# Optimization experiments

Measured on AMD Instinct MI355X. Metric: run time of the kernel, lower is better.

The kernel has to match this reference:

```python
import jax, jax.numpy as jnp
import numpy as np

IN_Q = 256   # in_features // 4
OUT_Q = 256  # out_features // 4


def setup_inputs() -> dict:
    key = jax.random.key(0)
    kx, kr, ki, kj, kk = jax.random.split(key, 5)
    stdv = 1.0 / np.sqrt(IN_Q)
    return {
        "x": jax.random.normal(kx, (4, 8192, IN_Q * 4), dtype=jnp.float32),
        "r_weight": jax.random.uniform(kr, (OUT_Q, IN_Q), minval=-stdv, maxval=stdv, dtype=jnp.float32),
        "i_weight": jax.random.uniform(ki, (OUT_Q, IN_Q), minval=-stdv, maxval=stdv, dtype=jnp.float32),
        "j_weight": jax.random.uniform(kj, (OUT_Q, IN_Q), minval=-stdv, maxval=stdv, dtype=jnp.float32),
        "k_weight": jax.random.uniform(kk, (OUT_Q, IN_Q), minval=-stdv, maxval=stdv, dtype=jnp.float32),
        "bias": jnp.zeros((OUT_Q * 4,), dtype=jnp.float32),
    }


def reference(x, r_weight, i_weight, j_weight, k_weight, bias):
    batch_dims = x.shape[:-1]
    xq = x.reshape(*batch_dims, IN_Q, 4)  # [..., in_q, 4]
    r_x, i_x, j_x, k_x = xq[..., 0], xq[..., 1], xq[..., 2], xq[..., 3]

    lin = lambda v, w: jnp.einsum('...i,oi->...o', v, w)  # F.linear, no bias

    out_r = lin(r_x, r_weight) - lin(i_x, i_weight) - lin(j_x, j_weight) - lin(k_x, k_weight)
    out_i = lin(r_x, i_weight) + lin(i_x, r_weight) + lin(j_x, k_weight) - lin(k_x, j_weight)
    out_j = lin(r_x, j_weight) - lin(i_x, k_weight) + lin(j_x, r_weight) + lin(k_x, i_weight)
    out_k = lin(r_x, k_weight) + lin(i_x, j_weight) - lin(j_x, i_weight) + lin(k_x, r_weight)

    out = jnp.stack([out_r, out_i, out_j, out_k], axis=-1)  # [..., out_q, 4]
    out = out.reshape(*batch_dims, OUT_Q * 4)
    return out + bias
```

## Files before the change

### kernel.cpp

```cpp
#include <hip/hip_runtime.h>


typedef __attribute__((ext_vector_type(8))) short bf16x8;
typedef __attribute__((ext_vector_type(4))) float f32x4;

#define M_TOT 32768
#define N_TOT 1024
#define K_TOT 1024
#define BM 128
#define BN 128
#define BK 32

__device__ __forceinline__ unsigned short f2bf(float f) {
    union { float f; unsigned int u; } v; v.f = f;
    unsigned int u = v.u;
    u += 0x7fffu + ((u >> 16) & 1u);
    return (unsigned short)(u >> 16);
}

__global__ __launch_bounds__(256) void cvt_x(const float4* __restrict__ x,
                                             ushort4* __restrict__ y) {
    int idx = blockIdx.x * 256 + threadIdx.x;
    float4 a = x[idx];
    ushort4 o;
    o.x = f2bf(a.x); o.y = f2bf(a.y); o.z = f2bf(a.z); o.w = f2bf(a.w);
    y[idx] = o;
}

__global__ __launch_bounds__(256) void build_w(const float* __restrict__ R,
                                               const float* __restrict__ I,
                                               const float* __restrict__ J,
                                               const float* __restrict__ Kw,
                                               ushort4* __restrict__ Wb) {
    int n = blockIdx.x;
    int i = threadIdx.x;
    int o = n >> 2, co = n & 3;
    int base = o * 256 + i;
    float r = R[base], ii = I[base], j = J[base], k = Kw[base];
    float v0, v1, v2, v3;
    if (co == 0)      { v0 = r;  v1 = -ii; v2 = -j;  v3 = -k; }
    else if (co == 1) { v0 = ii; v1 = r;   v2 = k;   v3 = -j; }
    else if (co == 2) { v0 = j;  v1 = -k;  v2 = r;   v3 = ii; }
    else              { v0 = k;  v1 = j;   v2 = -ii; v3 = r;  }
    ushort4 w;
    w.x = f2bf(v0); w.y = f2bf(v1); w.z = f2bf(v2); w.w = f2bf(v3);
    Wb[n * 256 + i] = w;
}

__device__ __forceinline__ void async_lds16(const void* g, void* l) {
    __builtin_amdgcn_global_load_lds(
        (const __attribute__((address_space(1))) unsigned int*)g,
        (__attribute__((address_space(3))) unsigned int*)l,
        16, 0, 0);
}

__global__ __launch_bounds__(256) void gemm_bt(
        const unsigned short* __restrict__ A,
        const unsigned short* __restrict__ B,
        const float* __restrict__ bias,
        float* __restrict__ C) {
    __shared__ unsigned short As[BM * BK];
    __shared__ unsigned short Bs[BN * BK];

    const int tid  = threadIdx.x;
    const int wave = tid >> 6;
    const int lane = tid & 63;
    const int quad = lane >> 4;
    const int r16  = lane & 15;
    const int wm   = wave & 1;
    const int wn   = wave >> 1;

    const int m0 = blockIdx.x * BM;
    const int n0 = blockIdx.y * BN;

    f32x4 acc[4][4];
#pragma unroll
    for (int i = 0; i < 4; ++i)
#pragma unroll
        for (int j = 0; j < 4; ++j)
            acc[i][j] = (f32x4){0.f, 0.f, 0.f, 0.f};

    const int srow = lane >> 2;
    const int scol = (lane & 3) * 8;

    for (int k0 = 0; k0 < K_TOT; k0 += BK) {
        __syncthreads();
#pragma unroll
        for (int j = 0; j < 2; ++j) {
            int q   = wave * 2 + j;
            int row = q * 16 + srow;
            async_lds16(A + (size_t)(m0 + row) * K_TOT + k0 + scol, As + q * 512);
            async_lds16(B + (size_t)(n0 + row) * K_TOT + k0 + scol, Bs + q * 512);
        }
        __syncthreads();

        bf16x8 af[4], bf[4];
#pragma unroll
        for (int i = 0; i < 4; ++i) {
            af[i] = *(const bf16x8*)(As + (wm * 64 + i * 16 + r16) * BK + quad * 8);
            bf[i] = *(const bf16x8*)(Bs + (wn * 64 + i * 16 + r16) * BK + quad * 8);
        }
#pragma unroll
        for (int i = 0; i < 4; ++i)
#pragma unroll
            for (int j = 0; j < 4; ++j)
                acc[i][j] = __builtin_amdgcn_mfma_f32_16x16x32_bf16(
                    af[i], bf[j], acc[i][j], 0, 0, 0);
    }

#pragma unroll
    for (int j = 0; j < 4; ++j) {
        int col  = n0 + wn * 64 + j * 16 + r16;
        float bv = bias[col];
#pragma unroll
        for (int i = 0; i < 4; ++i) {
            int rowb = m0 + wm * 64 + i * 16 + quad * 4;
            f32x4 v  = acc[i][j];
#pragma unroll
            for (int r = 0; r < 4; ++r)
                C[(size_t)(rowb + r) * N_TOT + col] = v[r] + bv;
        }
    }
}

extern "C" void kernel_launch(void* const* d_in, const int* in_sizes, int n_in,
                              void* d_out, int out_size, void* d_ws, size_t ws_size,
                              hipStream_t stream) {
    const float* x    = (const float*)d_in[0];
    const float* rw   = (const float*)d_in[1];
    const float* iw   = (const float*)d_in[2];
    const float* jw   = (const float*)d_in[3];
    const float* kw   = (const float*)d_in[4];
    const float* bias = (const float*)d_in[5];
    float* out = (float*)d_out;

    unsigned short* xb = (unsigned short*)d_ws;
    unsigned short* Wb = (unsigned short*)((char*)d_ws + (size_t)M_TOT * K_TOT * 2);

    cvt_x<<<(M_TOT * (size_t)K_TOT) / 4 / 256, 256, 0, stream>>>(
        (const float4*)x, (ushort4*)xb);

    build_w<<<N_TOT, 256, 0, stream>>>(rw, iw, jw, kw, (ushort4*)Wb);

    dim3 grid(M_TOT / BM, N_TOT / BN);
    gemm_bt<<<grid, 256, 0, stream>>>(xb, Wb, bias, out);
}
```

Baseline: 327.4 us.

## Rewrite GEMM as 256x256 double-buffered pipelined kernel with swizzled LDS

Replaces the 128x128x32 single-buffered GEMM with a 256x256x64 tile and 512 threads. LDS is double-buffered, with async global-to-LDS prefetch of the next K tiles interleaved between four MFMA phases. The LDS layout is XOR-swizzled to avoid bank conflicts, s_setprio prioritizes the MFMA sections, and a block-ID remap groups tiles for L2 reuse. The goal is to hide load latency and cut the per-tile barrier stalls. In exchange it adds heavy register pressure from 32 accumulators and intricate vmcnt/barrier bookkeeping that is hard to get right.

```diff
diff --git a/kernel.cpp b/kernel.cpp
--- a/kernel.cpp
+++ b/kernel.cpp
@@ -7,9 +7,10 @@
 #define M_TOT 32768
 #define N_TOT 1024
 #define K_TOT 1024
-#define BM 128
-#define BN 128
-#define BK 32
+#define BM 256
+#define BN 256
+#define BK 64
+#define NKT (K_TOT / BK)
 
 __device__ __forceinline__ unsigned short f2bf(float f) {
     union { float f; unsigned int u; } v; v.f = f;
@@ -54,13 +55,34 @@
         16, 0, 0);
 }
 
-__global__ __launch_bounds__(256) void gemm_bt(
+__device__ __forceinline__ void stage_ht(const unsigned short* __restrict__ G,
+                                         int row0, int k0,
+                                         unsigned short* ht,
+                                         int wave, int lane) {
+    int sr = lane >> 2;
+    int sc = ((lane & 3) * 8) ^ ((lane & 32) ? 16 : 0);
+#pragma unroll
+    for (int j = 0; j < 2; ++j) {
+        int si = j * 8 + wave;
+        int rg = si >> 1, cg = si & 1;
+        async_lds16(G + (size_t)(row0 + rg * 16 + sr) * K_TOT + k0 + cg * 32 + sc,
+                    ht + si * 512);
+    }
+}
+
+__device__ __forceinline__ bf16x8 frag_ld(const unsigned short* ht,
+                                          int row, int kk, int quad) {
+    int idx = (((row >> 4) << 1) + (kk >> 5)) * 512 + (row & 15) * 32 + quad * 8;
+    idx ^= (row & 8) << 1;
+    return *(const bf16x8*)(ht + idx);
+}
+
+__global__ __launch_bounds__(512, 2) void gemm_bt(
         const unsigned short* __restrict__ A,
         const unsigned short* __restrict__ B,
         const float* __restrict__ bias,
         float* __restrict__ C) {
-    __shared__ unsigned short As[BM * BK];
-    __shared__ unsigned short Bs[BN * BK];
+    __shared__ unsigned short smem[2][2][2][8192];
 
     const int tid  = threadIdx.x;
     const int wave = tid >> 6;
@@ -70,52 +92,140 @@
     const int wm   = wave & 1;
     const int wn   = wave >> 1;
 
-    const int m0 = blockIdx.x * BM;
-    const int n0 = blockIdx.y * BN;
-
-    f32x4 acc[4][4];
-#pragma unroll
-    for (int i = 0; i < 4; ++i)
+    int bid = blockIdx.x;
+    int wg  = (bid & 7) * 64 + (bid >> 3);
+    const int m0 = (wg >> 2) * BM;
+    const int n0 = (wg & 3) * BN;
+
+    f32x4 acc[8][4];
+#pragma unroll
+    for (int i = 0; i < 8; ++i)
 #pragma unroll
         for (int j = 0; j < 4; ++j)
             acc[i][j] = (f32x4){0.f, 0.f, 0.f, 0.f};
 
-    const int srow = lane >> 2;
-    const int scol = (lane & 3) * 8;
-
-    for (int k0 = 0; k0 < K_TOT; k0 += BK) {
-        __syncthreads();
-#pragma unroll
-        for (int j = 0; j < 2; ++j) {
-            int q   = wave * 2 + j;
-            int row = q * 16 + srow;
-            async_lds16(A + (size_t)(m0 + row) * K_TOT + k0 + scol, As + q * 512);
-            async_lds16(B + (size_t)(n0 + row) * K_TOT + k0 + scol, Bs + q * 512);
-        }
-        __syncthreads();
-
-        bf16x8 af[4], bf[4];
-#pragma unroll
-        for (int i = 0; i < 4; ++i) {
-            af[i] = *(const bf16x8*)(As + (wm * 64 + i * 16 + r16) * BK + quad * 8);
-            bf[i] = *(const bf16x8*)(Bs + (wn * 64 + i * 16 + r16) * BK + quad * 8);
-        }
-#pragma unroll
-        for (int i = 0; i < 4; ++i)
-#pragma unroll
-            for (int j = 0; j < 4; ++j)
-                acc[i][j] = __builtin_amdgcn_mfma_f32_16x16x32_bf16(
-                    af[i], bf[j], acc[i][j], 0, 0, 0);
+    const int brow0 = (wn & 1) * 64;
+
+    stage_ht(A, m0,        0, &smem[0][0][0][0], wave, lane);
+    stage_ht(A, m0 + 128,  0, &smem[0][0][1][0], wave, lane);
+    stage_ht(B, n0,        0, &smem[0][1][0][0], wave, lane);
+    stage_ht(B, n0 + 128,  0, &smem[0][1][1][0], wave, lane);
+    stage_ht(A, m0,       BK, &smem[1][0][0][0], wave, lane);
+    stage_ht(A, m0 + 128, BK, &smem[1][0][1][0], wave, lane);
+    asm volatile("s_waitcnt vmcnt(4)" ::: "memory");
+    __builtin_amdgcn_s_barrier();
+
+    bf16x8 af[4][2], bl[2][2], bh[2][2];
+
+#pragma unroll 2
+    for (int t = 0; t < NKT; ++t) {
+        const int c = t & 1;
+        const unsigned short* Ah = &smem[c][0][wm][0];
+        const unsigned short* Bh = &smem[c][1][wn >> 1][0];
+
+#pragma unroll
+        for (int mb = 0; mb < 4; ++mb) {
+            af[mb][0] = frag_ld(Ah, mb * 16 + r16, 0, quad);
+            af[mb][1] = frag_ld(Ah, mb * 16 + r16, 32, quad);
+        }
+#pragma unroll
+        for (int nb = 0; nb < 2; ++nb) {
+            bl[nb][0] = frag_ld(Bh, brow0 + nb * 16 + r16, 0, quad);
+            bl[nb][1] = frag_ld(Bh, brow0 + nb * 16 + r16, 32, quad);
+        }
+        if (t + 1 < NKT) {
+            stage_ht(B, n0,       (t + 1) * BK, &smem[c ^ 1][1][0][0], wave, lane);
+            stage_ht(B, n0 + 128, (t + 1) * BK, &smem[c ^ 1][1][1][0], wave, lane);
+        }
+        __builtin_amdgcn_s_barrier();
+        asm volatile("s_waitcnt lgkmcnt(0)" ::: "memory");
+        __builtin_amdgcn_s_setprio(1);
+#pragma unroll
+        for (int mb = 0; mb < 4; ++mb)
+#pragma unroll
+            for (int nb = 0; nb < 2; ++nb) {
+                acc[mb][nb] = __builtin_amdgcn_mfma_f32_16x16x32_bf16(
+                    af[mb][0], bl[nb][0], acc[mb][nb], 0, 0, 0);
+                acc[mb][nb] = __builtin_amdgcn_mfma_f32_16x16x32_bf16(
+                    af[mb][1], bl[nb][1], acc[mb][nb], 0, 0, 0);
+            }
+        __builtin_amdgcn_s_setprio(0);
+        __builtin_amdgcn_s_barrier();
+
+#pragma unroll
+        for (int nb = 0; nb < 2; ++nb) {
+            bh[nb][0] = frag_ld(Bh, brow0 + (nb + 2) * 16 + r16, 0, quad);
+            bh[nb][1] = frag_ld(Bh, brow0 + (nb + 2) * 16 + r16, 32, quad);
+        }
+        __builtin_amdgcn_s_barrier();
+        asm volatile("s_waitcnt lgkmcnt(0)" ::: "memory");
+        __builtin_amdgcn_s_setprio(1);
+#pragma unroll
+        for (int mb = 0; mb < 4; ++mb)
+#pragma unroll
+            for (int nb = 0; nb < 2; ++nb) {
+                acc[mb][nb + 2] = __builtin_amdgcn_mfma_f32_16x16x32_bf16(
+                    af[mb][0], bh[nb][0], acc[mb][nb + 2], 0, 0, 0);
+                acc[mb][nb + 2] = __builtin_amdgcn_mfma_f32_16x16x32_bf16(
+                    af[mb][1], bh[nb][1], acc[mb][nb + 2], 0, 0, 0);
+            }
+        __builtin_amdgcn_s_setprio(0);
+        __builtin_amdgcn_s_barrier();
+
+#pragma unroll
+        for (int mb = 0; mb < 4; ++mb) {
+            af[mb][0] = frag_ld(Ah, 64 + mb * 16 + r16, 0, quad);
+            af[mb][1] = frag_ld(Ah, 64 + mb * 16 + r16, 32, quad);
+        }
+        __builtin_amdgcn_s_barrier();
+        asm volatile("s_waitcnt lgkmcnt(0)" ::: "memory");
+        __builtin_amdgcn_s_setprio(1);
+#pragma unroll
+        for (int mb = 0; mb < 4; ++mb)
+#pragma unroll
+            for (int nb = 0; nb < 2; ++nb) {
+                acc[mb + 4][nb + 2] = __builtin_amdgcn_mfma_f32_16x16x32_bf16(
+                    af[mb][0], bh[nb][0], acc[mb + 4][nb + 2], 0, 0, 0);
+                acc[mb + 4][nb + 2] = __builtin_amdgcn_mfma_f32_16x16x32_bf16(
+                    af[mb][1], bh[nb][1], acc[mb + 4][nb + 2], 0, 0, 0);
+            }
+        __builtin_amdgcn_s_setprio(0);
+        __builtin_amdgcn_s_barrier();
+
+        if (t + 2 < NKT) {
+            stage_ht(A, m0,       (t + 2) * BK, &smem[c][0][0][0], wave, lane);
+            stage_ht(A, m0 + 128, (t + 2) * BK, &smem[c][0][1][0], wave, lane);
+        }
+        __builtin_amdgcn_s_barrier();
+        __builtin_amdgcn_s_setprio(1);
+#pragma unroll
+        for (int mb = 0; mb < 4; ++mb)
+#pragma unroll
+            for (int nb = 0; nb < 2; ++nb) {
+                acc[mb + 4][nb] = __builtin_amdgcn_mfma_f32_16x16x32_bf16(
+                    af[mb][0], bl[nb][0], acc[mb + 4][nb], 0, 0, 0);
+                acc[mb + 4][nb] = __builtin_amdgcn_mfma_f32_16x16x32_bf16(
+                    af[mb][1], bl[nb][1], acc[mb + 4][nb], 0, 0, 0);
+            }
+        __builtin_amdgcn_s_setprio(0);
+        if (t + 2 < NKT) {
+            asm volatile("s_waitcnt vmcnt(4)" ::: "memory");
+        } else if (t + 1 < NKT) {
+            asm volatile("s_waitcnt vmcnt(0)" ::: "memory");
+        }
+        __builtin_amdgcn_s_barrier();
     }
 
-#pragma unroll
-    for (int j = 0; j < 4; ++j) {
-        int col  = n0 + wn * 64 + j * 16 + r16;
+    const int mbase = m0 + wm * 128 + quad * 4;
+    const int nbase = n0 + wn * 64 + r16;
+#pragma unroll
+    for (int nb = 0; nb < 4; ++nb) {
+        int col  = nbase + nb * 16;
         float bv = bias[col];
 #pragma unroll
-        for (int i = 0; i < 4; ++i) {
-            int rowb = m0 + wm * 64 + i * 16 + quad * 4;
-            f32x4 v  = acc[i][j];
+        for (int mb = 0; mb < 8; ++mb) {
+            int rowb = mbase + mb * 16;
+            f32x4 v  = acc[mb][nb];
 #pragma unroll
             for (int r = 0; r < 4; ++r)
                 C[(size_t)(rowb + r) * N_TOT + col] = v[r] + bv;
@@ -142,6 +252,6 @@
 
     build_w<<<N_TOT, 256, 0, stream>>>(rw, iw, jw, kw, (ushort4*)Wb);
 
-    dim3 grid(M_TOT / BM, N_TOT / BN);
-    gemm_bt<<<grid, 256, 0, stream>>>(xb, Wb, bias, out);
-}
+    gemm_bt<<<dim3((M_TOT / BM) * (N_TOT / BN)), 512, 0, stream>>>(
+        xb, Wb, bias, out);
+}
```

New measurement: 324.9 us. No clear change (-0.8%).
